# Kernel tuning notes

Hardware: AMD Instinct MI355X
Metric: run time of the kernel (lower is better)

Reference implementation:

```python
import jax, jax.numpy as jnp
import numpy as np
from jax import lax

GAP_PENALTY = 0.0
TEMPERATURE = 1.0
B, A, L, D, K = 64, 26, 384, 512, 18


def setup_inputs() -> dict:
    key = jax.random.key(0)
    k1, k2, k3, k4 = jax.random.split(key, 4)
    matrices = jax.random.normal(k1, (B, A, L), dtype=jnp.float32)
    # ragged lengths: (len_i, len_0) per pair, in [L//2, L]
    shapes = jax.random.randint(k2, (B, 2), L // 2, L + 1, dtype=jnp.int32)
    s = 1.0 / np.sqrt(A * K)  # torch Conv1d default init scale
    conv_w = jax.random.uniform(k3, (D, A, K), minval=-s, maxval=s, dtype=jnp.float32)
    conv_b = jax.random.uniform(k4, (D,), minval=-s, maxval=s, dtype=jnp.float32)
    return {"matrices": matrices, "shapes": shapes, "conv_w": conv_w, "conv_b": conv_b}


def _smoothmax3(a, b, c, t):
    # t * log(exp(a/t) + exp(b/t) + exp(c/t)), numerically stable
    m = jnp.maximum(jnp.maximum(a, b), c)
    return m + t * jnp.log(jnp.exp((a - m) / t) + jnp.exp((b - m) / t) + jnp.exp((c - m) / t))


def _nw_matrix(sim, t, g):
    # sim: (L, L). Returns smoothed NW value matrix V: (L+1, L+1).
    # V[i,j] = sim[i-1,j-1] + smoothmax(V[i-1,j-1], V[i-1,j]-g, V[i,j-1]-g)
    n = sim.shape[0]
    row0 = -g * jnp.arange(n + 1, dtype=sim.dtype)  # free/affine leading gaps on top row

    def row_step(prev_row, inp):
        s_row, i = inp  # s_row: (L,)
        v_left0 = -g * i  # V[i, 0]

        def col_step(left, xs):
            s, diag, up = xs
            v = s + _smoothmax3(diag, up - g, left - g, t)
            return v, v

        _, rest = lax.scan(col_step, v_left0, (s_row, prev_row[:-1], prev_row[1:]))
        new_row = jnp.concatenate([v_left0[None], rest])
        return new_row, new_row

    _, rows = lax.scan(row_step, row0, (sim, jnp.arange(1, n + 1, dtype=sim.dtype)))
    return jnp.concatenate([row0[None], rows], axis=0)


def needleman_wunsch(sim, shapes, gap_penalty, temperature):
    # sim: (B, L, L) similarity vs sequence 0; shapes: (B, 2) int lengths.
    # Soft alignment posterior = grad of smoothed terminal score wrt similarity.
    li = jnp.clip(shapes[:, 0], 0, sim.shape[1])
    lj = jnp.clip(shapes[:, 1], 0, sim.shape[2])

    def total_score(s):
        V = jax.vmap(lambda m: _nw_matrix(m, temperature, gap_penalty))(s)  # (B, L+1, L+1)
        b = jnp.arange(s.shape[0])
        return jnp.sum(V[b, li, lj])

    return jax.grad(total_score)(sim)  # (B, L, L), expected match matrix


def reference(matrices, shapes, conv_w, conv_b):
    # Conv1d padding='same' with even kernel: torch pads (k-1)//2 left, k//2 right
    k = conv_w.shape[-1]
    pad = ((k - 1) // 2, k // 2)
    emb = lax.conv_general_dilated(
        matrices, conv_w, window_strides=(1,), padding=[pad],
        dimension_numbers=("NCH", "OIH", "NCH"),
    ) + conv_b[None, :, None]  # (B, D, L)
    e = jnp.transpose(emb, (0, 2, 1))  # (B, L, D)
    sim = jnp.einsum("bld,md->blm", e, e[0])  # (B, L_i, L_0): similarity vs sequence 0
    align = needleman_wunsch(sim, shapes, GAP_PENALTY, TEMPERATURE)  # (B, L, L)
    m = jnp.transpose(matrices, (0, 2, 1))  # (B, L, A)
    # consensus in sequence-0 coordinates, then project back to each sequence
    consensus = jnp.mean(jnp.einsum("nia,nij->nja", m, align), axis=0)  # (L, A)
    return jnp.einsum("ja,nij->nia", consensus, align)  # (B, L, A)
```

## Files before the change

kernel.cpp:

```cpp
#include <hip/hip_runtime.h>
#include <hip/hip_bf16.h>
#include <math.h>

#define B_  64
#define A_  26
#define L_  384
#define D_  512
#define K_  18
#define SZD 245760

typedef __attribute__((ext_vector_type(8))) short bf16x8;
typedef __attribute__((ext_vector_type(4))) float f32x4;
typedef unsigned short ushort_t;
typedef unsigned int uint_t;

__device__ __forceinline__ void stD(float* sp, int z, int c, float v) {
    int dl = z / 6, dr = z - dl * 6;
    sp[(size_t)(dl + (c >> 2)) * 1536 + dr * 256 + dl * 4 + (c & 3)] = v;
}

__device__ __forceinline__ ushort_t f2bf(float v) {
    uint_t u = __float_as_uint(v);
    uint_t r = (u + 0x7FFFu + ((u >> 16) & 1u)) >> 16;
    return (ushort_t)r;
}

__device__ __forceinline__ float dpp_up1(float x) {
    return __int_as_float(__builtin_amdgcn_update_dpp(
        0, __float_as_int(x), 0x138, 0xF, 0xF, true));
}
__device__ __forceinline__ float dpp_down1(float x) {
    return __int_as_float(__builtin_amdgcn_update_dpp(
        0, __float_as_int(x), 0x130, 0xF, 0xF, true));
}

__global__ void transpose_w_kernel(const float* __restrict__ w, float* __restrict__ wt) {
    int o = blockIdx.x * blockDim.x + threadIdx.x;
    int total = A_ * K_ * D_;
    if (o >= total) return;
    int d = o % D_;
    int r = o / D_;
    wt[o] = w[(size_t)d * (A_ * K_) + r];
}

__global__ __launch_bounds__(512) void conv_kernel(const float* __restrict__ x,
                                                   const float* __restrict__ wt,
                                                   const float* __restrict__ bias,
                                                   ushort_t* __restrict__ ehi,
                                                   ushort_t* __restrict__ elo) {
    const int TL = 32;
    const int XW = TL + K_ - 1;
    int l0 = blockIdx.x * TL;
    int b  = blockIdx.y;
    int d  = threadIdx.x;
    __shared__ float xs[A_][XW];
    for (int idx = threadIdx.x; idx < A_ * XW; idx += 512) {
        int a = idx / XW, p = idx % XW;
        int g = l0 - (K_ - 1) / 2 + p;
        xs[a][p] = (g >= 0 && g < L_) ? x[((size_t)b * A_ + a) * L_ + g] : 0.0f;
    }
    __syncthreads();
    float acc[TL];
#pragma unroll
    for (int l = 0; l < TL; ++l) acc[l] = 0.0f;
#pragma unroll 1
    for (int a = 0; a < A_; ++a) {
        float xr[XW];
#pragma unroll
        for (int p = 0; p < XW; ++p) xr[p] = xs[a][p];
        const float* wrow = wt + (size_t)(a * K_) * D_ + d;
#pragma unroll
        for (int k = 0; k < K_; ++k) {
            float w = wrow[(size_t)k * D_];
#pragma unroll
            for (int l = 0; l < TL; ++l)
                acc[l] = fmaf(xr[k + l], w, acc[l]);
        }
    }
    float bv = bias[d];
#pragma unroll
    for (int l = 0; l < TL; ++l) {
        float v = acc[l] + bv;
        ushort_t h = f2bf(v);
        float hf = __uint_as_float(((uint_t)h) << 16);
        ushort_t lo = f2bf(v - hf);
        size_t idx = ((size_t)b * L_ + (l0 + l)) * D_ + d;
        ehi[idx] = h;
        elo[idx] = lo;
    }
}

__global__ __launch_bounds__(256) void sim_kernel(const ushort_t* __restrict__ ehi,
                                                  const ushort_t* __restrict__ elo,
                                                  float* __restrict__ simD) {
    int b = blockIdx.z;
    int w = threadIdx.x >> 6;
    int lane = threadIdx.x & 63;
    int l0 = blockIdx.y * 64 + 32 * (w >> 1);
    int m0 = blockIdx.x * 64 + 32 * (w & 1);
    int r = lane & 15, g = lane >> 4;
    size_t rowA = ((size_t)b * L_ + l0 + r) * D_ + g * 8;
    size_t rowB = ((size_t)m0 + r) * D_ + g * 8;
    const ushort_t* pah = ehi + rowA;
    const ushort_t* pal = elo + rowA;
    const ushort_t* pbh = ehi + rowB;
    const ushort_t* pbl = elo + rowB;
    f32x4 acc00 = {0.f, 0.f, 0.f, 0.f}, acc01 = acc00, acc10 = acc00, acc11 = acc00;
#pragma unroll 2
    for (int ks = 0; ks < 16; ++ks) {
        int off = ks * 32;
        bf16x8 Ah0 = *(const bf16x8*)(pah + off);
        bf16x8 Ah1 = *(const bf16x8*)(pah + 16 * D_ + off);
        bf16x8 Al0 = *(const bf16x8*)(pal + off);
        bf16x8 Al1 = *(const bf16x8*)(pal + 16 * D_ + off);
        bf16x8 Bh0 = *(const bf16x8*)(pbh + off);
        bf16x8 Bh1 = *(const bf16x8*)(pbh + 16 * D_ + off);
        bf16x8 Bl0 = *(const bf16x8*)(pbl + off);
        bf16x8 Bl1 = *(const bf16x8*)(pbl + 16 * D_ + off);
        acc00 = __builtin_amdgcn_mfma_f32_16x16x32_bf16(Ah0, Bh0, acc00, 0, 0, 0);
        acc00 = __builtin_amdgcn_mfma_f32_16x16x32_bf16(Ah0, Bl0, acc00, 0, 0, 0);
        acc00 = __builtin_amdgcn_mfma_f32_16x16x32_bf16(Al0, Bh0, acc00, 0, 0, 0);
        acc01 = __builtin_amdgcn_mfma_f32_16x16x32_bf16(Ah0, Bh1, acc01, 0, 0, 0);
        acc01 = __builtin_amdgcn_mfma_f32_16x16x32_bf16(Ah0, Bl1, acc01, 0, 0, 0);
        acc01 = __builtin_amdgcn_mfma_f32_16x16x32_bf16(Al0, Bh1, acc01, 0, 0, 0);
        acc10 = __builtin_amdgcn_mfma_f32_16x16x32_bf16(Ah1, Bh0, acc10, 0, 0, 0);
        acc10 = __builtin_amdgcn_mfma_f32_16x16x32_bf16(Ah1, Bl0, acc10, 0, 0, 0);
        acc10 = __builtin_amdgcn_mfma_f32_16x16x32_bf16(Al1, Bh0, acc10, 0, 0, 0);
        acc11 = __builtin_amdgcn_mfma_f32_16x16x32_bf16(Ah1, Bh1, acc11, 0, 0, 0);
        acc11 = __builtin_amdgcn_mfma_f32_16x16x32_bf16(Ah1, Bl1, acc11, 0, 0, 0);
        acc11 = __builtin_amdgcn_mfma_f32_16x16x32_bf16(Al1, Bh1, acc11, 0, 0, 0);
    }
    float* sp = simD + (size_t)b * SZD;
#pragma unroll
    for (int v = 0; v < 4; ++v) {
        int ar0 = l0 + g * 4 + v, ar1 = ar0 + 16;
        int ac0 = m0 + r,         ac1 = ac0 + 16;
        stD(sp, ar0, ac0, acc00[v]);
        stD(sp, ar0, ac1, acc01[v]);
        stD(sp, ar1, ac0, acc10[v]);
        stD(sp, ar1, ac1, acc11[v]);
    }
}

__global__ __launch_bounds__(64, 1) void nw_fwd_kernel(const float* __restrict__ simD, float* __restrict__ VD) {
    int b = blockIdx.x;
    int l = threadIdx.x;
    const float* pS = simD + (size_t)b * SZD + l * 4;
    float*       pV = VD   + (size_t)b * SZD + l * 4;
    float vleft[6] = {0.f, 0.f, 0.f, 0.f, 0.f, 0.f};
    float bcarry[4] = {0.f, 0.f, 0.f, 0.f};
    float bprev = 0.f;

    auto body = [&](float4* buf, int Tb) {
        float sc[6][4];
#pragma unroll
        for (int r = 0; r < 6; ++r) {
            float4 t = buf[r];
            sc[r][0] = t.x; sc[r][1] = t.y; sc[r][2] = t.z; sc[r][3] = t.w;
        }
        int dP = min(Tb + 3, 158);
#pragma unroll
        for (int r = 0; r < 6; ++r) buf[r] = *(const float4*)(pS + dP * 1536 + r * 256);
        float d0 = dpp_up1(bprev);
        float uin[4];
#pragma unroll
        for (int q = 0; q < 4; ++q) uin[q] = dpp_up1(bcarry[q]);
        int c0 = 4 * (Tb - l);
        if (c0 >= 0 && c0 <= 380) {
            float vout[6][4];
#pragma unroll
            for (int q = 0; q < 4; ++q) {
                float dg = (q == 0) ? d0 : uin[q - 1];
                float up = uin[q];
#pragma unroll
                for (int r = 0; r < 6; ++r) {
                    float lf = vleft[r];
                    float mx = fmaxf(dg, fmaxf(up, lf));
                    float v = sc[r][q] + mx + __logf(__expf(dg - mx) + __expf(up - mx) + __expf(lf - mx));
                    dg = lf;
                    up = v;
                    vleft[r] = v;
                    vout[r][q] = v;
                }
            }
            bprev = bcarry[3];
#pragma unroll
            for (int q = 0; q < 4; ++q) bcarry[q] = vout[5][q];
#pragma unroll
            for (int r = 0; r < 6; ++r) {
                float4 t;
                t.x = vout[r][0]; t.y = vout[r][1]; t.z = vout[r][2]; t.w = vout[r][3];
                *(float4*)(pV + Tb * 1536 + r * 256) = t;
            }
        }
    };

    float4 buf0[6], buf1[6], buf2[6];
#pragma unroll
    for (int r = 0; r < 6; ++r) {
        buf0[r] = *(const float4*)(pS + 0 * 1536 + r * 256);
        buf1[r] = *(const float4*)(pS + 1 * 1536 + r * 256);
        buf2[r] = *(const float4*)(pS + 2 * 1536 + r * 256);
    }
#pragma unroll 1
    for (int Tb = 0; Tb < 159; Tb += 3) {
        body(buf0, Tb);
        body(buf1, Tb + 1);
        body(buf2, Tb + 2);
    }
}

__global__ __launch_bounds__(64, 1) void nw_bwd_kernel(const float* __restrict__ simD,
                                                       const float* __restrict__ VD,
                                                       const int* __restrict__ shapes,
                                                       float* __restrict__ ED) {
    int b = blockIdx.x;
    int l = threadIdx.x;
    const float* pS = simD + (size_t)b * SZD + l * 4;
    const float* pV = VD   + (size_t)b * SZD + l * 4;
    float*       pE = ED   + (size_t)b * SZD + l * 4;
    int li = min(max(shapes[2 * b + 0], 0), L_);
    int lj = min(max(shapes[2 * b + 1], 0), L_);
    float e[6] = {0.f, 0.f, 0.f, 0.f, 0.f, 0.f};
    float u[6] = {0.f, 0.f, 0.f, 0.f, 0.f, 0.f};
    float ecar[4] = {0.f, 0.f, 0.f, 0.f};
    float ucar[4] = {0.f, 0.f, 0.f, 0.f};
    float eprev_s = 0.f, uprev_s = 0.f;

    auto body = [&](float4* bufV, float4* bufS, int T) {
        float Vq[6][4], Sq[6][4];
#pragma unroll
        for (int r = 0; r < 6; ++r) {
            float4 tv = bufV[r], ts = bufS[r];
            Vq[r][0] = tv.x; Vq[r][1] = tv.y; Vq[r][2] = tv.z; Vq[r][3] = tv.w;
            Sq[r][0] = ts.x; Sq[r][1] = ts.y; Sq[r][2] = ts.z; Sq[r][3] = ts.w;
        }
        int dP = max(158 - T - 2, 0);
#pragma unroll
        for (int r = 0; r < 6; ++r) {
            bufV[r] = *(const float4*)(pV + dP * 1536 + r * 256);
            bufS[r] = *(const float4*)(pS + dP * 1536 + r * 256);
        }
        float enbtd_s = dpp_down1(eprev_s);
        float unbtd_s = dpp_down1(uprev_s);
        float enb_c[4], unb_c[4];
#pragma unroll
        for (int q = 0; q < 4; ++q) {
            enb_c[q] = dpp_down1(ecar[q]);
            unb_c[q] = dpp_down1(ucar[q]);
        }
        eprev_s = e[0]; uprev_s = u[0];
        int ct = 158 - T - l;
        if (ct >= 0 && ct <= 95) {
            float Eo[6][4];
#pragma unroll
            for (int qq = 0; qq < 4; ++qq) {
                const int q = 3 - qq;
                int j = 4 * ct + q + 1;
                bool jlt = (j < L_);
                float eo[6], uo[6];
#pragma unroll
                for (int r = 0; r < 6; ++r) { eo[r] = e[r]; uo[r] = u[r]; }
#pragma unroll
                for (int rr = 0; rr < 6; ++rr) {
                    const int r = 5 - rr;
                    int i = 6 * l + r + 1;
                    bool ilt = (i < L_);
                    float Vv = Vq[r][q];
                    float u_new = Vv - Sq[r][q];
                    float eb_old, ub_old, eb_new, ub_new;
                    if (r == 5) {
                        eb_old = (q == 3) ? enbtd_s : enb_c[q + 1];
                        ub_old = (q == 3) ? unbtd_s : unb_c[q + 1];
                        eb_new = enb_c[q];
                        ub_new = unb_c[q];
                    } else {
                        eb_old = eo[r + 1]; ub_old = uo[r + 1];
                        eb_new = e[r + 1];  ub_new = u[r + 1];
                    }
                    float wtd = (ilt && jlt) ? __expf(Vv - ub_old) : 0.f;
                    float wtu = ilt ? __expf(Vv - ub_new) : 0.f;
                    float wtl = jlt ? __expf(Vv - uo[r]) : 0.f;
                    float en = (i == li && j == lj) ? 1.f : 0.f;
                    en += wtd * eb_old + wtu * eb_new + wtl * eo[r];
                    e[r] = en; u[r] = u_new;
                    Eo[r][q] = en;
                }
            }
#pragma unroll
            for (int q = 0; q < 4; ++q) {
                ecar[q] = Eo[0][q];
                ucar[q] = Vq[0][q] - Sq[0][q];
            }
            float* pEd = pE + (size_t)(158 - T) * 1536;
#pragma unroll
            for (int r = 0; r < 6; ++r) {
                float4 t;
                t.x = Eo[r][0]; t.y = Eo[r][1]; t.z = Eo[r][2]; t.w = Eo[r][3];
                *(float4*)(pEd + r * 256) = t;
            }
        }
    };

    float4 bufVA[6], bufSA[6], bufVB[6], bufSB[6];
#pragma unroll
    for (int r = 0; r < 6; ++r) {
        bufVA[r] = *(const float4*)(pV + 158 * 1536 + r * 256);
        bufSA[r] = *(const float4*)(pS + 158 * 1536 + r * 256);
        bufVB[r] = *(const float4*)(pV + 157 * 1536 + r * 256);
        bufSB[r] = *(const float4*)(pS + 157 * 1536 + r * 256);
    }
#pragma unroll 1
    for (int T = 0; T < 160; T += 2) {
        body(bufVA, bufSA, T);
        body(bufVB, bufSB, T + 1);
    }
}

__global__ __launch_bounds__(256) void consensus_kernel(const float* __restrict__ x,
                                                        const float* __restrict__ ED,
                                                        float* __restrict__ cons) {
    int n  = blockIdx.y;
    int j0 = blockIdx.x * 64;
    __shared__ float ms[A_][L_];
    for (int idx = threadIdx.x; idx < A_ * L_; idx += 256)
        ((float*)ms)[idx] = x[(size_t)n * A_ * L_ + idx];
    __syncthreads();
    int jl = threadIdx.x & 63;
    int g  = threadIdx.x >> 6;
    int a0 = g * 7;
    int na = (a0 + 7 <= A_) ? 7 : (A_ - a0);
    int j  = j0 + jl;
    float acc[7] = {0.f, 0.f, 0.f, 0.f, 0.f, 0.f, 0.f};
    const float* aB = ED + (size_t)n * SZD + (j >> 2) * 1536 + (j & 3);
#pragma unroll 1
    for (int dl = 0; dl < 64; ++dl) {
        const float* ap = aB + dl * 1540;
#pragma unroll
        for (int dr = 0; dr < 6; ++dr) {
            float al = ap[dr * 256];
            int i = dl * 6 + dr;
#pragma unroll
            for (int t = 0; t < 7; ++t)
                if (t < na) acc[t] = fmaf(al, ms[a0 + t][i], acc[t]);
        }
    }
    for (int t = 0; t < na; ++t)
        atomicAdd(&cons[(size_t)j * A_ + a0 + t], acc[t] * (1.0f / B_));
}

__global__ __launch_bounds__(256) void out_kernel(const float* __restrict__ ED,
                                                  const float* __restrict__ cons,
                                                  float* __restrict__ out) {
    int n  = blockIdx.y;
    int i0 = blockIdx.x * 32;
    __shared__ float cs[L_][A_];
    __shared__ float as_[32][L_ + 1];
    for (int idx = threadIdx.x; idx < L_ * A_; idx += 256)
        ((float*)cs)[idx] = cons[idx];
    const float* aB = ED + (size_t)n * SZD;
    for (int idx = threadIdx.x; idx < 32 * L_; idx += 256) {
        int r = idx / L_, c = idx - r * L_;
        int z = i0 + r;
        int dl = z / 6, dr = z - dl * 6;
        as_[r][c] = aB[(size_t)(dl + (c >> 2)) * 1536 + dr * 256 + dl * 4 + (c & 3)];
    }
    __syncthreads();
    for (int o = threadIdx.x; o < 32 * A_; o += 256) {
        int il = o / A_, a = o % A_;
        float s = 0.f;
        for (int jj = 0; jj < L_; ++jj)
            s = fmaf(as_[il][jj], cs[jj][a], s);
        out[((size_t)n * L_ + i0 + il) * A_ + a] = s;
    }
}

extern "C" void kernel_launch(void* const* d_in, const int* in_sizes, int n_in,
                              void* d_out, int out_size, void* d_ws, size_t ws_size,
                              hipStream_t stream) {
    const float* matrices = (const float*)d_in[0];
    const int*   shapes   = (const int*)d_in[1];
    const float* conv_w   = (const float*)d_in[2];
    const float* conv_b   = (const float*)d_in[3];
    float* out = (float*)d_out;

    char* p = (char*)d_ws;
    float*    ED  = (float*)p;
    ushort_t* ehi = (ushort_t*)p;
    ushort_t* elo = ehi + (size_t)B_ * L_ * D_;
    float* simD = (float*)(p + (size_t)B_ * SZD * 4);
    float* VD   = simD + (size_t)B_ * SZD;
    float* wt   = VD + (size_t)B_ * SZD;
    float* cons = wt + (size_t)A_ * K_ * D_;

    transpose_w_kernel<<<(A_ * K_ * D_ + 255) / 256, 256, 0, stream>>>(conv_w, wt);
    conv_kernel<<<dim3(L_ / 32, B_), 512, 0, stream>>>(matrices, wt, conv_b, ehi, elo);
    sim_kernel<<<dim3(L_ / 64, L_ / 64, B_), 256, 0, stream>>>(ehi, elo, simD);
    nw_fwd_kernel<<<B_, 64, 0, stream>>>(simD, VD);
    nw_bwd_kernel<<<B_, 64, 0, stream>>>(simD, VD, shapes, ED);
    hipMemsetAsync(cons, 0, (size_t)L_ * A_ * sizeof(float), stream);
    consensus_kernel<<<dim3(L_ / 64, B_), 256, 0, stream>>>(matrices, ED, cons);
    out_kernel<<<dim3(L_ / 32, B_), 256, 0, stream>>>(ED, cons, out);
}
```

Baseline: 990.8 us.

## Round-robin NW wavefront steps across four waves with LDS flag handoff

The forward and backward soft Needleman-Wunsch kernels move from one 64-thread wave per batch to four waves per block. Consecutive anti-diagonal steps T are assigned to waves in round-robin order, and carried state passes between waves through LDS with spin-wait flags instead of DPP lane shifts inside one wave. The goal is to overlap each step's global loads, stores and instruction latency across waves so the serial dependency chain is less latency-bound. In exchange, every step now pays for LDS writes and reads, a waitcnt and a busy-wait, and the strict serial dependence between waves may cancel the overlap.

```diff
diff --git a/kernel.cpp b/kernel.cpp
--- a/kernel.cpp
+++ b/kernel.cpp
@@ -23,15 +23,6 @@
     uint_t u = __float_as_uint(v);
     uint_t r = (u + 0x7FFFu + ((u >> 16) & 1u)) >> 16;
     return (ushort_t)r;
-}
-
-__device__ __forceinline__ float dpp_up1(float x) {
-    return __int_as_float(__builtin_amdgcn_update_dpp(
-        0, __float_as_int(x), 0x138, 0xF, 0xF, true));
-}
-__device__ __forceinline__ float dpp_down1(float x) {
-    return __int_as_float(__builtin_amdgcn_update_dpp(
-        0, __float_as_int(x), 0x130, 0xF, 0xF, true));
 }
 
 __global__ void transpose_w_kernel(const float* __restrict__ w, float* __restrict__ wt) {
@@ -142,31 +133,51 @@
     }
 }
 
-__global__ __launch_bounds__(64, 1) void nw_fwd_kernel(const float* __restrict__ simD, float* __restrict__ VD) {
+__global__ __launch_bounds__(256, 1) void nw_fwd_kernel(const float* __restrict__ simD, float* __restrict__ VD) {
     int b = blockIdx.x;
-    int l = threadIdx.x;
+    int tid = threadIdx.x;
+    int w = tid >> 6, l = tid & 63;
+    __shared__ float4 MA[4][64], MB4[4][64], MC[4][64];
+    __shared__ int FL[4];
+    const float4 Z4 = {0.f, 0.f, 0.f, 0.f};
+    for (int k = tid; k < 256; k += 256) {
+        int s = k >> 6, ll = k & 63;
+        MA[s][ll] = Z4; MB4[s][ll] = Z4; MC[s][ll] = Z4;
+    }
+    if (tid < 4) FL[tid] = (tid == 3) ? -1 : -1000000;
+    __syncthreads();
+    volatile int* flg = FL;
     const float* pS = simD + (size_t)b * SZD + l * 4;
     float*       pV = VD   + (size_t)b * SZD + l * 4;
-    float vleft[6] = {0.f, 0.f, 0.f, 0.f, 0.f, 0.f};
-    float bcarry[4] = {0.f, 0.f, 0.f, 0.f};
-    float bprev = 0.f;
-
-    auto body = [&](float4* buf, int Tb) {
+    float4 buf[6];
+#pragma unroll
+    for (int r = 0; r < 6; ++r) buf[r] = *(const float4*)(pS + w * 1536 + r * 256);
+    int lm = (l == 0) ? 0 : (l - 1);
+#pragma unroll 1
+    for (int T = w; T < 159; T += 4) {
+        int sp = (T - 1) & 3;
+        while (flg[sp] != T - 1) {}
+        asm volatile("" ::: "memory");
+        float4 Ar = MA[sp][l];
+        float4 Bs = MB4[sp][l];
+        float4 Cs = MC[sp][l];
+        float4 Bn = MB4[sp][lm];
+        float4 Cn = MC[sp][lm];
+        if (l == 0) { Bn = Z4; Cn = Z4; }
+        float vleft[6] = {Ar.x, Ar.y, Ar.z, Ar.w, Bs.x, Bs.y};
+        float d0 = Bn.z;
+        float uin[4] = {Cn.x, Cn.y, Cn.z, Cn.w};
         float sc[6][4];
 #pragma unroll
         for (int r = 0; r < 6; ++r) {
-            float4 t = buf[r];
-            sc[r][0] = t.x; sc[r][1] = t.y; sc[r][2] = t.z; sc[r][3] = t.w;
-        }
-        int dP = min(Tb + 3, 158);
+            sc[r][0] = buf[r].x; sc[r][1] = buf[r].y; sc[r][2] = buf[r].z; sc[r][3] = buf[r].w;
+        }
+        int dP = min(T + 4, 158);
 #pragma unroll
         for (int r = 0; r < 6; ++r) buf[r] = *(const float4*)(pS + dP * 1536 + r * 256);
-        float d0 = dpp_up1(bprev);
-        float uin[4];
-#pragma unroll
-        for (int q = 0; q < 4; ++q) uin[q] = dpp_up1(bcarry[q]);
-        int c0 = 4 * (Tb - l);
-        if (c0 >= 0 && c0 <= 380) {
+        int ct = T - l;
+        float nbc[4] = {0.f, 0.f, 0.f, 0.f}, nbp = 0.f;
+        if (ct >= 0 && ct <= 95) {
             float vout[6][4];
 #pragma unroll
             for (int q = 0; q < 4; ++q) {
@@ -177,80 +188,93 @@
                     float lf = vleft[r];
                     float mx = fmaxf(dg, fmaxf(up, lf));
                     float v = sc[r][q] + mx + __logf(__expf(dg - mx) + __expf(up - mx) + __expf(lf - mx));
-                    dg = lf;
-                    up = v;
+                    dg = lf; up = v;
                     vleft[r] = v;
                     vout[r][q] = v;
                 }
             }
-            bprev = bcarry[3];
-#pragma unroll
-            for (int q = 0; q < 4; ++q) bcarry[q] = vout[5][q];
+            nbp = Cs.w;
+#pragma unroll
+            for (int q = 0; q < 4; ++q) nbc[q] = vout[5][q];
+            float* pVd = pV + (size_t)T * 1536;
 #pragma unroll
             for (int r = 0; r < 6; ++r) {
                 float4 t;
                 t.x = vout[r][0]; t.y = vout[r][1]; t.z = vout[r][2]; t.w = vout[r][3];
-                *(float4*)(pV + Tb * 1536 + r * 256) = t;
+                *(float4*)(pVd + r * 256) = t;
             }
         }
-    };
-
-    float4 buf0[6], buf1[6], buf2[6];
-#pragma unroll
-    for (int r = 0; r < 6; ++r) {
-        buf0[r] = *(const float4*)(pS + 0 * 1536 + r * 256);
-        buf1[r] = *(const float4*)(pS + 1 * 1536 + r * 256);
-        buf2[r] = *(const float4*)(pS + 2 * 1536 + r * 256);
-    }
-#pragma unroll 1
-    for (int Tb = 0; Tb < 159; Tb += 3) {
-        body(buf0, Tb);
-        body(buf1, Tb + 1);
-        body(buf2, Tb + 2);
-    }
-}
-
-__global__ __launch_bounds__(64, 1) void nw_bwd_kernel(const float* __restrict__ simD,
-                                                       const float* __restrict__ VD,
-                                                       const int* __restrict__ shapes,
-                                                       float* __restrict__ ED) {
+        float4 pa; pa.x = vleft[0]; pa.y = vleft[1]; pa.z = vleft[2]; pa.w = vleft[3];
+        float4 pb; pb.x = vleft[4]; pb.y = vleft[5]; pb.z = nbp; pb.w = 0.f;
+        float4 pc; pc.x = nbc[0]; pc.y = nbc[1]; pc.z = nbc[2]; pc.w = nbc[3];
+        MA[w][l] = pa; MB4[w][l] = pb; MC[w][l] = pc;
+        asm volatile("s_waitcnt lgkmcnt(0)" ::: "memory");
+        if (l == 0) flg[w] = T;
+    }
+}
+
+__global__ __launch_bounds__(256, 1) void nw_bwd_kernel(const float* __restrict__ simD,
+                                                        const float* __restrict__ VD,
+                                                        const int* __restrict__ shapes,
+                                                        float* __restrict__ ED) {
     int b = blockIdx.x;
-    int l = threadIdx.x;
+    int tid = threadIdx.x;
+    int w = tid >> 6, l = tid & 63;
+    __shared__ float4 MA[4][64], MB4[4][64], MC[4][64], MD[4][64], MEx[4][64], MF[4][64];
+    __shared__ int FL[4];
+    const float4 Z4 = {0.f, 0.f, 0.f, 0.f};
+    for (int k = tid; k < 256; k += 256) {
+        int s = k >> 6, ll = k & 63;
+        MA[s][ll] = Z4; MB4[s][ll] = Z4; MC[s][ll] = Z4;
+        MD[s][ll] = Z4; MEx[s][ll] = Z4; MF[s][ll] = Z4;
+    }
+    if (tid < 4) FL[tid] = (tid == 3) ? -1 : -1000000;
+    __syncthreads();
+    volatile int* flg = FL;
     const float* pS = simD + (size_t)b * SZD + l * 4;
     const float* pV = VD   + (size_t)b * SZD + l * 4;
     float*       pE = ED   + (size_t)b * SZD + l * 4;
     int li = min(max(shapes[2 * b + 0], 0), L_);
     int lj = min(max(shapes[2 * b + 1], 0), L_);
-    float e[6] = {0.f, 0.f, 0.f, 0.f, 0.f, 0.f};
-    float u[6] = {0.f, 0.f, 0.f, 0.f, 0.f, 0.f};
-    float ecar[4] = {0.f, 0.f, 0.f, 0.f};
-    float ucar[4] = {0.f, 0.f, 0.f, 0.f};
-    float eprev_s = 0.f, uprev_s = 0.f;
-
-    auto body = [&](float4* bufV, float4* bufS, int T) {
+    float4 bufV[6], bufS[6];
+#pragma unroll
+    for (int r = 0; r < 6; ++r) {
+        bufV[r] = *(const float4*)(pV + (158 - w) * 1536 + r * 256);
+        bufS[r] = *(const float4*)(pS + (158 - w) * 1536 + r * 256);
+    }
+    int lp = (l == 63) ? 63 : (l + 1);
+#pragma unroll 1
+    for (int T = w; T < 159; T += 4) {
+        int sp = (T - 1) & 3;
+        while (flg[sp] != T - 1) {}
+        asm volatile("" ::: "memory");
+        float4 Ar = MA[sp][l];
+        float4 Br = MB4[sp][l];
+        float4 Cr = MC[sp][l];
+        float4 Dn = MD[sp][lp];
+        float4 En = MEx[sp][lp];
+        float4 Fn = MF[sp][lp];
+        if (l == 63) { Dn = Z4; En = Z4; Fn = Z4; }
+        float e[6] = {Ar.x, Ar.y, Ar.z, Ar.w, Br.x, Br.y};
+        float u[6] = {Br.z, Br.w, Cr.x, Cr.y, Cr.z, Cr.w};
+        float enb_c[4] = {Dn.x, Dn.y, Dn.z, Dn.w};
+        float unb_c[4] = {En.x, En.y, En.z, En.w};
+        float enbtd_s = Fn.x, unbtd_s = Fn.y;
+        float e0r = e[0], u0r = u[0];
         float Vq[6][4], Sq[6][4];
 #pragma unroll
         for (int r = 0; r < 6; ++r) {
-            float4 tv = bufV[r], ts = bufS[r];
-            Vq[r][0] = tv.x; Vq[r][1] = tv.y; Vq[r][2] = tv.z; Vq[r][3] = tv.w;
-            Sq[r][0] = ts.x; Sq[r][1] = ts.y; Sq[r][2] = ts.z; Sq[r][3] = ts.w;
-        }
-        int dP = max(158 - T - 2, 0);
+            Vq[r][0] = bufV[r].x; Vq[r][1] = bufV[r].y; Vq[r][2] = bufV[r].z; Vq[r][3] = bufV[r].w;
+            Sq[r][0] = bufS[r].x; Sq[r][1] = bufS[r].y; Sq[r][2] = bufS[r].z; Sq[r][3] = bufS[r].w;
+        }
+        int dP = max(158 - (T + 4), 0);
 #pragma unroll
         for (int r = 0; r < 6; ++r) {
             bufV[r] = *(const float4*)(pV + dP * 1536 + r * 256);
             bufS[r] = *(const float4*)(pS + dP * 1536 + r * 256);
         }
-        float enbtd_s = dpp_down1(eprev_s);
-        float unbtd_s = dpp_down1(uprev_s);
-        float enb_c[4], unb_c[4];
-#pragma unroll
-        for (int q = 0; q < 4; ++q) {
-            enb_c[q] = dpp_down1(ecar[q]);
-            unb_c[q] = dpp_down1(ucar[q]);
-        }
-        eprev_s = e[0]; uprev_s = u[0];
         int ct = 158 - T - l;
+        float necar[4] = {0.f, 0.f, 0.f, 0.f}, nucar[4] = {0.f, 0.f, 0.f, 0.f};
         if (ct >= 0 && ct <= 95) {
             float Eo[6][4];
 #pragma unroll
@@ -289,8 +313,8 @@
             }
 #pragma unroll
             for (int q = 0; q < 4; ++q) {
-                ecar[q] = Eo[0][q];
-                ucar[q] = Vq[0][q] - Sq[0][q];
+                necar[q] = Eo[0][q];
+                nucar[q] = Vq[0][q] - Sq[0][q];
             }
             float* pEd = pE + (size_t)(158 - T) * 1536;
 #pragma unroll
@@ -300,20 +324,16 @@
                 *(float4*)(pEd + r * 256) = t;
             }
         }
-    };
-
-    float4 bufVA[6], bufSA[6], bufVB[6], bufSB[6];
-#pragma unroll
-    for (int r = 0; r < 6; ++r) {
-        bufVA[r] = *(const float4*)(pV + 158 * 1536 + r * 256);
-        bufSA[r] = *(const float4*)(pS + 158 * 1536 + r * 256);
-        bufVB[r] = *(const float4*)(pV + 157 * 1536 + r * 256);
-        bufSB[r] = *(const float4*)(pS + 157 * 1536 + r * 256);
-    }
-#pragma unroll 1
-    for (int T = 0; T < 160; T += 2) {
-        body(bufVA, bufSA, T);
-        body(bufVB, bufSB, T + 1);
+        float4 pa; pa.x = e[0]; pa.y = e[1]; pa.z = e[2]; pa.w = e[3];
+        float4 pb; pb.x = e[4]; pb.y = e[5]; pb.z = u[0]; pb.w = u[1];
+        float4 pc; pc.x = u[2]; pc.y = u[3]; pc.z = u[4]; pc.w = u[5];
+        float4 pd; pd.x = necar[0]; pd.y = necar[1]; pd.z = necar[2]; pd.w = necar[3];
+        float4 pe; pe.x = nucar[0]; pe.y = nucar[1]; pe.z = nucar[2]; pe.w = nucar[3];
+        float4 pf; pf.x = e0r; pf.y = u0r; pf.z = 0.f; pf.w = 0.f;
+        MA[w][l] = pa; MB4[w][l] = pb; MC[w][l] = pc;
+        MD[w][l] = pd; MEx[w][l] = pe; MF[w][l] = pf;
+        asm volatile("s_waitcnt lgkmcnt(0)" ::: "memory");
+        if (l == 0) flg[w] = T;
     }
 }
 
@@ -396,8 +416,8 @@
     transpose_w_kernel<<<(A_ * K_ * D_ + 255) / 256, 256, 0, stream>>>(conv_w, wt);
     conv_kernel<<<dim3(L_ / 32, B_), 512, 0, stream>>>(matrices, wt, conv_b, ehi, elo);
     sim_kernel<<<dim3(L_ / 64, L_ / 64, B_), 256, 0, stream>>>(ehi, elo, simD);
-    nw_fwd_kernel<<<B_, 64, 0, stream>>>(simD, VD);
-    nw_bwd_kernel<<<B_, 64, 0, stream>>>(simD, VD, shapes, ED);
+    nw_fwd_kernel<<<B_, 256, 0, stream>>>(simD, VD);
+    nw_bwd_kernel<<<B_, 256, 0, stream>>>(simD, VD, shapes, ED);
     hipMemsetAsync(cons, 0, (size_t)L_ * A_ * sizeof(float), stream);
     consensus_kernel<<<dim3(L_ / 64, B_), 256, 0, stream>>>(matrices, ED, cons);
     out_kernel<<<dim3(L_ / 32, B_), 256, 0, stream>>>(ED, cons, out);
```

Result: no change. 988.6 us (-0.2%).
